# Kernel optimization log

Hardware: AMD Instinct MI355X
Metric: run time of the kernel (lower is better)

Reference implementation:

```python
import jax, jax.numpy as jnp
import numpy as np

N, C, H, W = 4, 256, 64, 64  # in_channels == out_channels == C


def conv1x1(x, w, b):
    # x: [N, Cin, H, W], w: [Cout, Cin], b: [Cout]
    return jnp.einsum('nchw,oc->nohw', x, w) + b[None, :, None, None]


def setup_inputs() -> dict:
    key = jax.random.key(0)
    ks = jax.random.split(key, 4)
    scale = 1.0 / np.sqrt(C)
    return {
        'x': jax.random.normal(ks[0], (N, C, H, W), dtype=jnp.float32),
        'theta_w': jax.random.normal(ks[1], (C, C), dtype=jnp.float32) * scale,
        'theta_b': jnp.zeros((C,), dtype=jnp.float32),
        'phi_w': jax.random.normal(ks[2], (C, C), dtype=jnp.float32) * scale,
        'phi_b': jnp.zeros((C,), dtype=jnp.float32),
        'conv1_w': jax.random.normal(ks[3], (C, C), dtype=jnp.float32) * scale,
        'conv1_b': jnp.zeros((C,), dtype=jnp.float32),
    }


def reference(x, theta_w, theta_b, phi_w, phi_b, conv1_w, conv1_b):
    n, c, h, w = x.shape
    hw = h * w
    theta = conv1x1(x, theta_w, theta_b).reshape(n, c, hw)   # queries [N,C,HW]
    phi = conv1x1(x, phi_w, phi_b).reshape(n, c, hw)         # keys    [N,C,HW]
    g = x.reshape(n, c, hw)                                   # values  [N,C,HW]
    # f = einsum('niab,nicd->nabcd') flattened: [N, HW_q, HW_k]
    scores = jnp.einsum('ncp,ncq->npq', theta, phi) / jnp.sqrt(jnp.asarray(c, x.dtype))
    attn = jax.nn.softmax(scores, axis=-1)                    # softmax over keys
    # f = einsum('nabcd,nicd->niab'): weighted sum of values
    f = jnp.einsum('npq,ncq->ncp', attn, g).reshape(n, c, h, w)
    result = conv1x1(f, conv1_w, conv1_b)
    return x + result
```

## Files before the change

kernel.cpp:

```cpp
#include <hip/hip_runtime.h>
#include <hip/hip_bf16.h>

typedef __attribute__((ext_vector_type(8))) short short8;
typedef __attribute__((ext_vector_type(4))) short short4_t;
typedef __attribute__((ext_vector_type(4))) float float4_t;
typedef unsigned short ushort;

#define HW 4096
#define CC 256
#define NBATCH 4
#define SEQ ((size_t)NBATCH * HW)

static __device__ __forceinline__ unsigned short f2b(float f) {
    union { float f; unsigned u; } v; v.f = f;
    unsigned r = v.u + 0x7FFF + ((v.u >> 16) & 1);
    return (unsigned short)(r >> 16);
}
static __device__ __forceinline__ float b2f(unsigned short u) {
    union { unsigned u; float f; } v; v.u = ((unsigned)u) << 16;
    return v.f;
}
static __device__ __forceinline__ unsigned pk2(float a, float b) {
    __hip_bfloat162 h = __float22bfloat162_rn(make_float2(a, b));
    union { __hip_bfloat162 h; unsigned u; } v; v.h = h; return v.u;
}

__global__ __launch_bounds__(512)
void k_pp(const float* __restrict__ x,
          const float* __restrict__ tw, const float* __restrict__ pw,
          const float* __restrict__ thb, const float* __restrict__ phb,
          unsigned short* __restrict__ gb,
          unsigned short* __restrict__ thT, unsigned short* __restrict__ phT) {
    __shared__ float T[64][65];
    __shared__ __align__(16) ushort F[64][256];
    const int n = blockIdx.z;
    const int p0 = blockIdx.x * 64;
    const int tid = threadIdx.x;

    {
        const int pl = tid & 63, rg = tid >> 6;
        for (int cc = 0; cc < 4; cc++) {
            const int c0 = cc * 64;
            const float* xp = x + ((size_t)n * CC + c0) * HW + p0;
            #pragma unroll
            for (int i = 0; i < 8; i++) {
                int cl = rg * 8 + i;
                float v = xp[(size_t)cl * HW + pl];
                T[cl][pl] = v;
                gb[((size_t)n * CC + c0 + cl) * HW + p0 + pl] = f2b(v);
            }
            __syncthreads();
            const int cl2 = tid & 63, pg = tid >> 6;
            #pragma unroll
            for (int i = 0; i < 8; i++) {
                int plw = pg * 8 + i;
                int c = c0 + cl2;
                int swz = (c >> 3) ^ (plw & 7);
                F[plw][swz * 8 + (c & 7)] = f2b(T[cl2][plw]);
            }
            __syncthreads();
        }
    }

    const int w = tid >> 6, lane = tid & 63;
    const int nidx = lane & 15, quad = lane >> 4;
    const float* Wsel = (w < 4) ? tw : pw;
    const float* bsel = (w < 4) ? thb : phb;
    unsigned short* osel = (w < 4) ? thT : phT;
    const int cq = w & 3;

    float4_t acc[4][4];
    #pragma unroll
    for (int i = 0; i < 4; i++)
        #pragma unroll
        for (int j = 0; j < 4; j++) acc[i][j] = (float4_t)(0.f);

    for (int ks = 0; ks < 8; ks++) {
        short8 af[4];
        #pragma unroll
        for (int mt = 0; mt < 4; mt++) {
            int row = mt * 16 + nidx;
            int chn = (ks * 4 + quad) ^ (row & 7);
            af[mt] = *(const short8*)(&F[row][chn * 8]);
        }
        #pragma unroll
        for (int cb = 0; cb < 4; cb++) {
            int co = cq * 64 + cb * 16 + nidx;
            const float* wp = Wsel + (size_t)co * CC + ks * 32 + quad * 8;
            float4_t w0 = *(const float4_t*)(wp);
            float4_t w1 = *(const float4_t*)(wp + 4);
            union { short8 s; unsigned u[4]; } bfr;
            bfr.u[0] = pk2(w0[0], w0[1]); bfr.u[1] = pk2(w0[2], w0[3]);
            bfr.u[2] = pk2(w1[0], w1[1]); bfr.u[3] = pk2(w1[2], w1[3]);
            #pragma unroll
            for (int mt = 0; mt < 4; mt++)
                acc[mt][cb] = __builtin_amdgcn_mfma_f32_16x16x32_bf16(af[mt], bfr.s, acc[mt][cb], 0, 0, 0);
        }
    }

    #pragma unroll
    for (int cb = 0; cb < 4; cb++) {
        int co = cq * 64 + cb * 16 + nidx;
        float bias = bsel[co];
        #pragma unroll
        for (int mt = 0; mt < 4; mt++)
            #pragma unroll
            for (int r = 0; r < 4; r++) {
                size_t prow = (size_t)n * HW + p0 + mt * 16 + quad * 4 + r;
                osel[prow * CC + co] = f2b(acc[mt][cb][r] + bias);
            }
    }
}

__global__ __launch_bounds__(512)
void k_attn(const unsigned short* __restrict__ thetaT,
            const unsigned short* __restrict__ phiT,
            const unsigned short* __restrict__ gb,
            ushort* __restrict__ Ow, float* __restrict__ lw) {
    __shared__ __align__(16) ushort Kl[2][16384];
    __shared__ __align__(16) ushort Pbuf[2][16][64][8];
    __shared__ float Lbuf[2][128];

    const int tid = threadIdx.x;
    const int w = tid >> 6, lane = tid & 63;
    const int nidx = lane & 15, quad = lane >> 4;
    const int qg = w & 3;
    const int kh = w >> 2;
    const int nb = (blockIdx.x & 7) >> 1;
    const int h  = blockIdx.x & 1;
    const int qtile = blockIdx.x >> 3;
    const int p0 = qtile * 128;
    const size_t seq0 = (size_t)nb * HW;
    const ushort* Kg = phiT + seq0 * CC;
    const ushort* Vg = gb + (size_t)nb * CC * HW;
    const int k00 = h * 2048;

    short8 th[2][8];
    #pragma unroll
    for (int qs = 0; qs < 2; qs++) {
        const ushort* qrow = thetaT + (seq0 + p0 + qg * 32 + qs * 16 + nidx) * CC + quad * 8;
        #pragma unroll
        for (int kb = 0; kb < 8; kb++) th[qs][kb] = *(const short8*)(qrow + kb * 32);
    }

    float4_t o[2][8];
    #pragma unroll
    for (int i = 0; i < 2; i++)
        #pragma unroll
        for (int j = 0; j < 8; j++) o[i][j] = (float4_t)(0.f);
    float lrow[2] = {0.f, 0.f};

    const int c_s = tid >> 4, n_s = tid & 15;
    const int kfbase = (c_s >> 2) * 512 + ((c_s & 3) * 16 + n_s) * 8;
    auto loadKregs = [&](short8 (&kr)[4], int tt) {
        #pragma unroll
        for (int rr = 0; rr < 4; rr++)
            kr[rr] = *(const short8*)(Kg + (size_t)(k00 + tt * 64 + rr * 16 + n_s) * CC + c_s * 8);
    };
    auto stageK = [&](int buf, const short8 (&kr)[4]) {
        #pragma unroll
        for (int rr = 0; rr < 4; rr++) *(short8*)(&Kl[buf][rr * 4096 + kfbase]) = kr[rr];
    };
    auto loadVregs = [&](short8 (&vr)[4], int tt) {
        #pragma unroll
        for (int mg = 0; mg < 2; mg++)
            #pragma unroll
            for (int kst = 0; kst < 2; kst++)
                vr[mg * 2 + kst] = *(const short8*)(Vg + (size_t)(w * 32 + mg * 16 + nidx) * HW
                                                    + k00 + tt * 64 + kst * 32 + quad * 8);
    };

    const float SC = 0.0625f * 1.44269504088896f;
    const int Gp = quad >> 1;
    const int pcell_lo = (nidx ^ (Gp * 4));
    const int pj0 = (quad & 1) * 4;
    const int prcell = ((lane >> 4) << 4) | ((lane & 15) ^ (((lane >> 4) & 1) * 4));

    float4_t s00, s01, s10, s11;
    auto expPhase = [&](int buf) {
        {
            float e0 = exp2f(s00[0] * SC), e1 = exp2f(s00[1] * SC);
            float e2 = exp2f(s00[2] * SC), e3 = exp2f(s00[3] * SC);
            lrow[0] += (e0 + e1) + (e2 + e3);
            uint2 pk; pk.x = pk2(e0, e1); pk.y = pk2(e2, e3);
            *(uint2*)(&Pbuf[buf][(qg * 2 + 0) * 2 + kh][(0 * 2 + Gp) * 16 + pcell_lo][pj0]) = pk;
        }
        {
            float e0 = exp2f(s01[0] * SC), e1 = exp2f(s01[1] * SC);
            float e2 = exp2f(s01[2] * SC), e3 = exp2f(s01[3] * SC);
            lrow[1] += (e0 + e1) + (e2 + e3);
            uint2 pk; pk.x = pk2(e0, e1); pk.y = pk2(e2, e3);
            *(uint2*)(&Pbuf[buf][(qg * 2 + 1) * 2 + kh][(0 * 2 + Gp) * 16 + pcell_lo][pj0]) = pk;
        }
        {
            float e0 = exp2f(s10[0] * SC), e1 = exp2f(s10[1] * SC);
            float e2 = exp2f(s10[2] * SC), e3 = exp2f(s10[3] * SC);
            lrow[0] += (e0 + e1) + (e2 + e3);
            uint2 pk; pk.x = pk2(e0, e1); pk.y = pk2(e2, e3);
            *(uint2*)(&Pbuf[buf][(qg * 2 + 0) * 2 + kh][(1 * 2 + Gp) * 16 + pcell_lo][pj0]) = pk;
        }
        {
            float e0 = exp2f(s11[0] * SC), e1 = exp2f(s11[1] * SC);
            float e2 = exp2f(s11[2] * SC), e3 = exp2f(s11[3] * SC);
            lrow[1] += (e0 + e1) + (e2 + e3);
            uint2 pk; pk.x = pk2(e0, e1); pk.y = pk2(e2, e3);
            *(uint2*)(&Pbuf[buf][(qg * 2 + 1) * 2 + kh][(1 * 2 + Gp) * 16 + pcell_lo][pj0]) = pk;
        }
    };

    short8 kregs[4], vA[4], vB[4];

    auto ITER = [&](int t, const short8 (&vCur)[4], short8 (&vNext)[4]) {
        const int pb = t & 1;
        const int kbuf = (t + 1) & 1;
        s00 = (float4_t)(0.f); s01 = (float4_t)(0.f);
        s10 = (float4_t)(0.f); s11 = (float4_t)(0.f);
        #pragma unroll
        for (int i = 0; i < 8; i++) {
            short8 k0 = *(const short8*)(&Kl[kbuf][((kh * 2 + 0) * 8 + i) * 512 + lane * 8]);
            short8 k1 = *(const short8*)(&Kl[kbuf][((kh * 2 + 1) * 8 + i) * 512 + lane * 8]);
            s00 = __builtin_amdgcn_mfma_f32_16x16x32_bf16(k0, th[0][i], s00, 0, 0, 0);
            s01 = __builtin_amdgcn_mfma_f32_16x16x32_bf16(k0, th[1][i], s01, 0, 0, 0);
            s10 = __builtin_amdgcn_mfma_f32_16x16x32_bf16(k1, th[0][i], s10, 0, 0, 0);
            s11 = __builtin_amdgcn_mfma_f32_16x16x32_bf16(k1, th[1][i], s11, 0, 0, 0);
            short8 pf0 = *(const short8*)(&Pbuf[pb][i * 2 + 0][prcell][0]);
            short8 pf1 = *(const short8*)(&Pbuf[pb][i * 2 + 1][prcell][0]);
            o[0][i] = __builtin_amdgcn_mfma_f32_16x16x32_bf16(vCur[0], pf0, o[0][i], 0, 0, 0);
            o[0][i] = __builtin_amdgcn_mfma_f32_16x16x32_bf16(vCur[1], pf1, o[0][i], 0, 0, 0);
            o[1][i] = __builtin_amdgcn_mfma_f32_16x16x32_bf16(vCur[2], pf0, o[1][i], 0, 0, 0);
            o[1][i] = __builtin_amdgcn_mfma_f32_16x16x32_bf16(vCur[3], pf1, o[1][i], 0, 0, 0);
        }
        loadVregs(vNext, t + 1);
        expPhase((t + 1) & 1);
        if (t < 30) {
            stageK((t + 2) & 1, kregs);
            loadKregs(kregs, (t + 3 < 32) ? t + 3 : 31);
        }
        __syncthreads();
    };

    loadKregs(kregs, 0); loadVregs(vA, 0);
    stageK(0, kregs);
    loadKregs(kregs, 1);
    __syncthreads();
    s00 = (float4_t)(0.f); s01 = (float4_t)(0.f); s10 = (float4_t)(0.f); s11 = (float4_t)(0.f);
    #pragma unroll
    for (int kb = 0; kb < 8; kb++) {
        short8 k0 = *(const short8*)(&Kl[0][((kh * 2 + 0) * 8 + kb) * 512 + lane * 8]);
        short8 k1 = *(const short8*)(&Kl[0][((kh * 2 + 1) * 8 + kb) * 512 + lane * 8]);
        s00 = __builtin_amdgcn_mfma_f32_16x16x32_bf16(k0, th[0][kb], s00, 0, 0, 0);
        s01 = __builtin_amdgcn_mfma_f32_16x16x32_bf16(k0, th[1][kb], s01, 0, 0, 0);
        s10 = __builtin_amdgcn_mfma_f32_16x16x32_bf16(k1, th[0][kb], s10, 0, 0, 0);
        s11 = __builtin_amdgcn_mfma_f32_16x16x32_bf16(k1, th[1][kb], s11, 0, 0, 0);
    }
    expPhase(0);
    stageK(1, kregs);
    loadKregs(kregs, 2);
    __syncthreads();

    #pragma unroll 1
    for (int tt = 0; tt < 15; tt++) {
        ITER(tt * 2, vA, vB);
        ITER(tt * 2 + 1, vB, vA);
    }
    ITER(30, vA, vB);
    #pragma unroll
    for (int i = 0; i < 8; i++) {
        short8 pf0 = *(const short8*)(&Pbuf[1][i * 2 + 0][prcell][0]);
        short8 pf1 = *(const short8*)(&Pbuf[1][i * 2 + 1][prcell][0]);
        o[0][i] = __builtin_amdgcn_mfma_f32_16x16x32_bf16(vB[0], pf0, o[0][i], 0, 0, 0);
        o[0][i] = __builtin_amdgcn_mfma_f32_16x16x32_bf16(vB[1], pf1, o[0][i], 0, 0, 0);
        o[1][i] = __builtin_amdgcn_mfma_f32_16x16x32_bf16(vB[2], pf0, o[1][i], 0, 0, 0);
        o[1][i] = __builtin_amdgcn_mfma_f32_16x16x32_bf16(vB[3], pf1, o[1][i], 0, 0, 0);
    }

    #pragma unroll
    for (int qs = 0; qs < 2; qs++) {
        float v = lrow[qs];
        v += __shfl_xor(v, 16);
        v += __shfl_xor(v, 32);
        if (quad == 0) Lbuf[kh][qg * 32 + qs * 16 + nidx] = v;
    }
    __syncthreads();
    if (tid < 128)
        lw[(size_t)h * SEQ + seq0 + p0 + tid] = Lbuf[0][tid] + Lbuf[1][tid];
    ushort* Op = Ow + ((size_t)h * SEQ + seq0 + p0) * CC;
    #pragma unroll
    for (int mg = 0; mg < 2; mg++)
        #pragma unroll
        for (int qq = 0; qq < 8; qq++) {
            uint2 pk;
            pk.x = pk2(o[mg][qq][0], o[mg][qq][1]);
            pk.y = pk2(o[mg][qq][2], o[mg][qq][3]);
            *(uint2*)(Op + (size_t)(qq * 16 + nidx) * CC + w * 32 + mg * 16 + quad * 4) = pk;
        }
}

__global__ __launch_bounds__(512)
void k_final(const float* __restrict__ cw,
             const float* __restrict__ bc,
             const ushort* __restrict__ Ow,
             const float* __restrict__ lw,
             const float* __restrict__ x,
             float* __restrict__ out) {
    __shared__ __align__(16) ushort F[64][256];
    const int n = blockIdx.z;
    const int p0 = blockIdx.x * 64;
    const int tid = threadIdx.x;

    {
        const int r = tid >> 3;
        const int c0 = tid & 7;
        const size_t grow = (size_t)n * HW + p0 + r;
        const float li = 1.0f / (lw[grow] + lw[SEQ + grow]);
        const short8* O0 = (const short8*)(Ow + grow * CC);
        const short8* O1 = (const short8*)(Ow + SEQ * CC + grow * CC);
        #pragma unroll
        for (int i = 0; i < 4; i++) {
            int ch = c0 + 8 * i;
            short8 a = O0[ch];
            short8 b = O1[ch];
            union { short8 s; unsigned u[4]; } pk;
            float f[8];
            #pragma unroll
            for (int j = 0; j < 8; j++)
                f[j] = (b2f((ushort)a[j]) + b2f((ushort)b[j])) * li;
            pk.u[0] = pk2(f[0], f[1]); pk.u[1] = pk2(f[2], f[3]);
            pk.u[2] = pk2(f[4], f[5]); pk.u[3] = pk2(f[6], f[7]);
            int swz = ch ^ (r & 7);
            *(short8*)(&F[r][swz * 8]) = pk.s;
        }
    }
    __syncthreads();

    const int w = tid >> 6, lane = tid & 63;
    const int nidx = lane & 15, quad = lane >> 4;
    const int co_base = w * 32;
    float4_t acc[2][4];
    #pragma unroll
    for (int i = 0; i < 2; i++)
        #pragma unroll
        for (int j = 0; j < 4; j++) acc[i][j] = (float4_t)(0.f);

    const float* a0row = cw + (size_t)(co_base + nidx) * CC + quad * 8;
    const float* a1row = cw + (size_t)(co_base + 16 + nidx) * CC + quad * 8;
    for (int ks = 0; ks < 8; ks++) {
        float4_t w00 = *(const float4_t*)(a0row + ks * 32);
        float4_t w01 = *(const float4_t*)(a0row + ks * 32 + 4);
        float4_t w10 = *(const float4_t*)(a1row + ks * 32);
        float4_t w11 = *(const float4_t*)(a1row + ks * 32 + 4);
        union { short8 s; unsigned u[4]; } a0, a1;
        a0.u[0] = pk2(w00[0], w00[1]); a0.u[1] = pk2(w00[2], w00[3]);
        a0.u[2] = pk2(w01[0], w01[1]); a0.u[3] = pk2(w01[2], w01[3]);
        a1.u[0] = pk2(w10[0], w10[1]); a1.u[1] = pk2(w10[2], w10[3]);
        a1.u[2] = pk2(w11[0], w11[1]); a1.u[3] = pk2(w11[2], w11[3]);
        #pragma unroll
        for (int pb = 0; pb < 4; pb++) {
            int row = pb * 16 + nidx;
            int chunk = (ks * 4 + quad) ^ (row & 7);
            short8 bb = *(const short8*)(&F[row][chunk * 8]);
            acc[0][pb] = __builtin_amdgcn_mfma_f32_16x16x32_bf16(a0.s, bb, acc[0][pb], 0, 0, 0);
            acc[1][pb] = __builtin_amdgcn_mfma_f32_16x16x32_bf16(a1.s, bb, acc[1][pb], 0, 0, 0);
        }
    }

    #pragma unroll
    for (int cb = 0; cb < 2; cb++) {
        #pragma unroll
        for (int pb = 0; pb < 4; pb++) {
            #pragma unroll
            for (int r2 = 0; r2 < 4; r2++) {
                int co = co_base + cb * 16 + quad * 4 + r2;
                size_t idx = ((size_t)n * CC + co) * HW + p0 + pb * 16 + nidx;
                out[idx] = x[idx] + bc[co] + acc[cb][pb][r2];
            }
        }
    }
}

extern "C" void kernel_launch(void* const* d_in, const int* in_sizes, int n_in,
                              void* d_out, int out_size, void* d_ws, size_t ws_size,
                              hipStream_t stream) {
    const float* x       = (const float*)d_in[0];
    const float* theta_w = (const float*)d_in[1];
    const float* theta_b = (const float*)d_in[2];
    const float* phi_w   = (const float*)d_in[3];
    const float* phi_b   = (const float*)d_in[4];
    const float* conv1_w = (const float*)d_in[5];
    const float* conv1_b = (const float*)d_in[6];
    float* out = (float*)d_out;

    unsigned short* gb  = (unsigned short*)d_ws;
    unsigned short* thT = gb  + SEQ * CC;
    unsigned short* phT = thT + SEQ * CC;
    unsigned short* Ow  = phT + SEQ * CC;
    float* lw = (float*)(Ow + 2 * SEQ * CC);

    k_pp<<<dim3(64, 1, 4), 512, 0, stream>>>(x, theta_w, phi_w, theta_b, phi_b, gb, thT, phT);
    k_attn<<<dim3(256), 512, 0, stream>>>(thT, phT, gb, Ow, lw);
    k_final<<<dim3(64, 1, 4), 512, 0, stream>>>(conv1_w, conv1_b, Ow, lw, x, out);
}
```

Before: 185.1 us.

## Merge three kernels into one cooperative kernel with grid syncs

```diff
diff --git a/kernel.cpp b/kernel.cpp
--- a/kernel.cpp
+++ b/kernel.cpp
@@ -1,8 +1,10 @@
 #include <hip/hip_runtime.h>
 #include <hip/hip_bf16.h>
+#include <hip/hip_cooperative_groups.h>
+
+namespace cg = cooperative_groups;
 
 typedef __attribute__((ext_vector_type(8))) short short8;
-typedef __attribute__((ext_vector_type(4))) short short4_t;
 typedef __attribute__((ext_vector_type(4))) float float4_t;
 typedef unsigned short ushort;
 
@@ -25,354 +27,373 @@
     union { __hip_bfloat162 h; unsigned u; } v; v.h = h; return v.u;
 }
 
+struct SmemAttn {
+    ushort Kl[2][16384];
+    ushort Pbuf[2][16][64][8];
+    float  Lbuf[2][128];
+};
+struct SmemPp {
+    float  T[64][65];
+    ushort F[64][256];
+};
+struct SmemFin {
+    ushort F[64][256];
+};
+union SmemU {
+    SmemAttn a;
+    SmemPp   p;
+    SmemFin  f;
+};
+
 __global__ __launch_bounds__(512)
-void k_pp(const float* __restrict__ x,
-          const float* __restrict__ tw, const float* __restrict__ pw,
-          const float* __restrict__ thb, const float* __restrict__ phb,
-          unsigned short* __restrict__ gb,
-          unsigned short* __restrict__ thT, unsigned short* __restrict__ phT) {
-    __shared__ float T[64][65];
-    __shared__ __align__(16) ushort F[64][256];
-    const int n = blockIdx.z;
-    const int p0 = blockIdx.x * 64;
+void k_mega(const float* __restrict__ x,
+            const float* __restrict__ tw, const float* __restrict__ pw,
+            const float* __restrict__ thb, const float* __restrict__ phb,
+            const float* __restrict__ cw, const float* __restrict__ cbias,
+            unsigned short* __restrict__ gb,
+            unsigned short* __restrict__ thT, unsigned short* __restrict__ phT,
+            ushort* __restrict__ Ow, float* __restrict__ lw,
+            float* __restrict__ out) {
+    __shared__ __align__(16) SmemU sm;
+    cg::grid_group grid = cg::this_grid();
+    const int bid = blockIdx.x;
     const int tid = threadIdx.x;
 
     {
-        const int pl = tid & 63, rg = tid >> 6;
-        for (int cc = 0; cc < 4; cc++) {
-            const int c0 = cc * 64;
-            const float* xp = x + ((size_t)n * CC + c0) * HW + p0;
-            #pragma unroll
-            for (int i = 0; i < 8; i++) {
-                int cl = rg * 8 + i;
-                float v = xp[(size_t)cl * HW + pl];
-                T[cl][pl] = v;
-                gb[((size_t)n * CC + c0 + cl) * HW + p0 + pl] = f2b(v);
-            }
-            __syncthreads();
-            const int cl2 = tid & 63, pg = tid >> 6;
-            #pragma unroll
-            for (int i = 0; i < 8; i++) {
-                int plw = pg * 8 + i;
-                int c = c0 + cl2;
-                int swz = (c >> 3) ^ (plw & 7);
-                F[plw][swz * 8 + (c & 7)] = f2b(T[cl2][plw]);
-            }
-            __syncthreads();
-        }
-    }
-
-    const int w = tid >> 6, lane = tid & 63;
-    const int nidx = lane & 15, quad = lane >> 4;
-    const float* Wsel = (w < 4) ? tw : pw;
-    const float* bsel = (w < 4) ? thb : phb;
-    unsigned short* osel = (w < 4) ? thT : phT;
-    const int cq = w & 3;
-
-    float4_t acc[4][4];
-    #pragma unroll
-    for (int i = 0; i < 4; i++)
-        #pragma unroll
-        for (int j = 0; j < 4; j++) acc[i][j] = (float4_t)(0.f);
-
-    for (int ks = 0; ks < 8; ks++) {
-        short8 af[4];
-        #pragma unroll
-        for (int mt = 0; mt < 4; mt++) {
-            int row = mt * 16 + nidx;
-            int chn = (ks * 4 + quad) ^ (row & 7);
-            af[mt] = *(const short8*)(&F[row][chn * 8]);
-        }
+        auto& T = sm.p.T;
+        auto& F = sm.p.F;
+        const int n = bid >> 6;
+        const int p0 = (bid & 63) * 64;
+
+        {
+            const int pl = tid & 63, rg = tid >> 6;
+            for (int cc = 0; cc < 4; cc++) {
+                const int c0 = cc * 64;
+                const float* xp = x + ((size_t)n * CC + c0) * HW + p0;
+                #pragma unroll
+                for (int i = 0; i < 8; i++) {
+                    int cl = rg * 8 + i;
+                    float v = xp[(size_t)cl * HW + pl];
+                    T[cl][pl] = v;
+                    gb[((size_t)n * CC + c0 + cl) * HW + p0 + pl] = f2b(v);
+                }
+                __syncthreads();
+                const int cl2 = tid & 63, pg = tid >> 6;
+                #pragma unroll
+                for (int i = 0; i < 8; i++) {
+                    int plw = pg * 8 + i;
+                    int c = c0 + cl2;
+                    int swz = (c >> 3) ^ (plw & 7);
+                    F[plw][swz * 8 + (c & 7)] = f2b(T[cl2][plw]);
+                }
+                __syncthreads();
+            }
+        }
+
+        const int w = tid >> 6, lane = tid & 63;
+        const int nidx = lane & 15, quad = lane >> 4;
+        const float* Wsel = (w < 4) ? tw : pw;
+        const float* bsel = (w < 4) ? thb : phb;
+        unsigned short* osel = (w < 4) ? thT : phT;
+        const int cq = w & 3;
+
+        float4_t acc[4][4];
+        #pragma unroll
+        for (int i = 0; i < 4; i++)
+            #pragma unroll
+            for (int j = 0; j < 4; j++) acc[i][j] = (float4_t)(0.f);
+
+        for (int ks = 0; ks < 8; ks++) {
+            short8 af[4];
+            #pragma unroll
+            for (int mt = 0; mt < 4; mt++) {
+                int row = mt * 16 + nidx;
+                int chn = (ks * 4 + quad) ^ (row & 7);
+                af[mt] = *(const short8*)(&F[row][chn * 8]);
+            }
+            #pragma unroll
+            for (int cb = 0; cb < 4; cb++) {
+                int co = cq * 64 + cb * 16 + nidx;
+                const float* wp = Wsel + (size_t)co * CC + ks * 32 + quad * 8;
+                float4_t w0 = *(const float4_t*)(wp);
+                float4_t w1 = *(const float4_t*)(wp + 4);
+                union { short8 s; unsigned u[4]; } bfr;
+                bfr.u[0] = pk2(w0[0], w0[1]); bfr.u[1] = pk2(w0[2], w0[3]);
+                bfr.u[2] = pk2(w1[0], w1[1]); bfr.u[3] = pk2(w1[2], w1[3]);
+                #pragma unroll
+                for (int mt = 0; mt < 4; mt++)
+                    acc[mt][cb] = __builtin_amdgcn_mfma_f32_16x16x32_bf16(af[mt], bfr.s, acc[mt][cb], 0, 0, 0);
+            }
+        }
+
         #pragma unroll
         for (int cb = 0; cb < 4; cb++) {
             int co = cq * 64 + cb * 16 + nidx;
-            const float* wp = Wsel + (size_t)co * CC + ks * 32 + quad * 8;
-            float4_t w0 = *(const float4_t*)(wp);
-            float4_t w1 = *(const float4_t*)(wp + 4);
-            union { short8 s; unsigned u[4]; } bfr;
-            bfr.u[0] = pk2(w0[0], w0[1]); bfr.u[1] = pk2(w0[2], w0[3]);
-            bfr.u[2] = pk2(w1[0], w1[1]); bfr.u[3] = pk2(w1[2], w1[3]);
+            float bias = bsel[co];
             #pragma unroll
             for (int mt = 0; mt < 4; mt++)
-                acc[mt][cb] = __builtin_amdgcn_mfma_f32_16x16x32_bf16(af[mt], bfr.s, acc[mt][cb], 0, 0, 0);
+                #pragma unroll
+                for (int r = 0; r < 4; r++) {
+                    size_t prow = (size_t)n * HW + p0 + mt * 16 + quad * 4 + r;
+                    osel[prow * CC + co] = f2b(acc[mt][cb][r] + bias);
+                }
         }
     }
 
-    #pragma unroll
-    for (int cb = 0; cb < 4; cb++) {
-        int co = cq * 64 + cb * 16 + nidx;
-        float bias = bsel[co];
-        #pragma unroll
-        for (int mt = 0; mt < 4; mt++)
-            #pragma unroll
-            for (int r = 0; r < 4; r++) {
-                size_t prow = (size_t)n * HW + p0 + mt * 16 + quad * 4 + r;
-                osel[prow * CC + co] = f2b(acc[mt][cb][r] + bias);
+    grid.sync();
+
+    {
+        auto& Kl = sm.a.Kl;
+        auto& Pbuf = sm.a.Pbuf;
+        auto& Lbuf = sm.a.Lbuf;
+
+        const int w = tid >> 6, lane = tid & 63;
+        const int nidx = lane & 15, quad = lane >> 4;
+        const int qg = w & 3;
+        const int kh = w >> 2;
+        const int nb = (bid & 7) >> 1;
+        const int h  = bid & 1;
+        const int qtile = bid >> 3;
+        const int p0 = qtile * 128;
+        const size_t seq0 = (size_t)nb * HW;
+        const ushort* Kg = phT + seq0 * CC;
+        const ushort* Vg = gb + (size_t)nb * CC * HW;
+        const int k00 = h * 2048;
+
+        short8 th[2][8];
+        #pragma unroll
+        for (int qs = 0; qs < 2; qs++) {
+            const ushort* qrow = thT + (seq0 + p0 + qg * 32 + qs * 16 + nidx) * CC + quad * 8;
+            #pragma unroll
+            for (int kb = 0; kb < 8; kb++) th[qs][kb] = *(const short8*)(qrow + kb * 32);
+        }
+
+        float4_t o[2][8];
+        #pragma unroll
+        for (int i = 0; i < 2; i++)
+            #pragma unroll
+            for (int j = 0; j < 8; j++) o[i][j] = (float4_t)(0.f);
+        float lrow[2] = {0.f, 0.f};
+
+        const int c_s = tid >> 4, n_s = tid & 15;
+        const int kfbase = (c_s >> 2) * 512 + ((c_s & 3) * 16 + n_s) * 8;
+        auto loadKregs = [&](short8 (&kr)[4], int tt) {
+            #pragma unroll
+            for (int rr = 0; rr < 4; rr++)
+                kr[rr] = *(const short8*)(Kg + (size_t)(k00 + tt * 64 + rr * 16 + n_s) * CC + c_s * 8);
+        };
+        auto stageK = [&](int buf, const short8 (&kr)[4]) {
+            #pragma unroll
+            for (int rr = 0; rr < 4; rr++) *(short8*)(&Kl[buf][rr * 4096 + kfbase]) = kr[rr];
+        };
+        auto loadVregs = [&](short8 (&vr)[4], int tt) {
+            #pragma unroll
+            for (int mg = 0; mg < 2; mg++)
+                #pragma unroll
+                for (int kst = 0; kst < 2; kst++)
+                    vr[mg * 2 + kst] = *(const short8*)(Vg + (size_t)(w * 32 + mg * 16 + nidx) * HW
+                                                        + k00 + tt * 64 + kst * 32 + quad * 8);
+        };
+
+        const float SC = 0.0625f * 1.44269504088896f;
+        const int Gp = quad >> 1;
+        const int pcell_lo = (nidx ^ (Gp * 4));
+        const int pj0 = (quad & 1) * 4;
+        const int prcell = ((lane >> 4) << 4) | ((lane & 15) ^ (((lane >> 4) & 1) * 4));
+
+        float4_t s00, s01, s10, s11;
+        auto expPhase = [&](int buf) {
+            {
+                float e0 = exp2f(s00[0] * SC), e1 = exp2f(s00[1] * SC);
+                float e2 = exp2f(s00[2] * SC), e3 = exp2f(s00[3] * SC);
+                lrow[0] += (e0 + e1) + (e2 + e3);
+                uint2 pk; pk.x = pk2(e0, e1); pk.y = pk2(e2, e3);
+                *(uint2*)(&Pbuf[buf][(qg * 2 + 0) * 2 + kh][(0 * 2 + Gp) * 16 + pcell_lo][pj0]) = pk;
+            }
+            {
+                float e0 = exp2f(s01[0] * SC), e1 = exp2f(s01[1] * SC);
+                float e2 = exp2f(s01[2] * SC), e3 = exp2f(s01[3] * SC);
+                lrow[1] += (e0 + e1) + (e2 + e3);
+                uint2 pk; pk.x = pk2(e0, e1); pk.y = pk2(e2, e3);
+                *(uint2*)(&Pbuf[buf][(qg * 2 + 1) * 2 + kh][(0 * 2 + Gp) * 16 + pcell_lo][pj0]) = pk;
+            }
+            {
+                float e0 = exp2f(s10[0] * SC), e1 = exp2f(s10[1] * SC);
+                float e2 = exp2f(s10[2] * SC), e3 = exp2f(s10[3] * SC);
+                lrow[0] += (e0 + e1) + (e2 + e3);
+                uint2 pk; pk.x = pk2(e0, e1); pk.y = pk2(e2, e3);
+                *(uint2*)(&Pbuf[buf][(qg * 2 + 0) * 2 + kh][(1 * 2 + Gp) * 16 + pcell_lo][pj0]) = pk;
+            }
+            {
+                float e0 = exp2f(s11[0] * SC), e1 = exp2f(s11[1] * SC);
+                float e2 = exp2f(s11[2] * SC), e3 = exp2f(s11[3] * SC);
+                lrow[1] += (e0 + e1) + (e2 + e3);
+                uint2 pk; pk.x = pk2(e0, e1); pk.y = pk2(e2, e3);
+                *(uint2*)(&Pbuf[buf][(qg * 2 + 1) * 2 + kh][(1 * 2 + Gp) * 16 + pcell_lo][pj0]) = pk;
+            }
+        };
+
+        short8 kregs[4], vA[4], vB[4];
+
+        auto ITER = [&](int t, const short8 (&vCur)[4], short8 (&vNext)[4]) {
+            const int pb = t & 1;
+            const int kbuf = (t + 1) & 1;
+            s00 = (float4_t)(0.f); s01 = (float4_t)(0.f);
+            s10 = (float4_t)(0.f); s11 = (float4_t)(0.f);
+            #pragma unroll
+            for (int i = 0; i < 8; i++) {
+                short8 k0 = *(const short8*)(&Kl[kbuf][((kh * 2 + 0) * 8 + i) * 512 + lane * 8]);
+                short8 k1 = *(const short8*)(&Kl[kbuf][((kh * 2 + 1) * 8 + i) * 512 + lane * 8]);
+                s00 = __builtin_amdgcn_mfma_f32_16x16x32_bf16(k0, th[0][i], s00, 0, 0, 0);
+                s01 = __builtin_amdgcn_mfma_f32_16x16x32_bf16(k0, th[1][i], s01, 0, 0, 0);
+                s10 = __builtin_amdgcn_mfma_f32_16x16x32_bf16(k1, th[0][i], s10, 0, 0, 0);
+                s11 = __builtin_amdgcn_mfma_f32_16x16x32_bf16(k1, th[1][i], s11, 0, 0, 0);
+                short8 pf0 = *(const short8*)(&Pbuf[pb][i * 2 + 0][prcell][0]);
+                short8 pf1 = *(const short8*)(&Pbuf[pb][i * 2 + 1][prcell][0]);
+                o[0][i] = __builtin_amdgcn_mfma_f32_16x16x32_bf16(vCur[0], pf0, o[0][i], 0, 0, 0);
+                o[0][i] = __builtin_amdgcn_mfma_f32_16x16x32_bf16(vCur[1], pf1, o[0][i], 0, 0, 0);
+                o[1][i] = __builtin_amdgcn_mfma_f32_16x16x32_bf16(vCur[2], pf0, o[1][i], 0, 0, 0);
+                o[1][i] = __builtin_amdgcn_mfma_f32_16x16x32_bf16(vCur[3], pf1, o[1][i], 0, 0, 0);
+            }
+            loadVregs(vNext, t + 1);
+            expPhase((t + 1) & 1);
+            if (t < 30) {
+                stageK((t + 2) & 1, kregs);
+                loadKregs(kregs, (t + 3 < 32) ? t + 3 : 31);
+            }
+            __syncthreads();
+        };
+
+        loadKregs(kregs, 0); loadVregs(vA, 0);
+        stageK(0, kregs);
+        loadKregs(kregs, 1);
+        __syncthreads();
+        s00 = (float4_t)(0.f); s01 = (float4_t)(0.f); s10 = (float4_t)(0.f); s11 = (float4_t)(0.f);
+        #pragma unroll
+        for (int kb = 0; kb < 8; kb++) {
+            short8 k0 = *(const short8*)(&Kl[0][((kh * 2 + 0) * 8 + kb) * 512 + lane * 8]);
+            short8 k1 = *(const short8*)(&Kl[0][((kh * 2 + 1) * 8 + kb) * 512 + lane * 8]);
+            s00 = __builtin_amdgcn_mfma_f32_16x16x32_bf16(k0, th[0][kb], s00, 0, 0, 0);
+            s01 = __builtin_amdgcn_mfma_f32_16x16x32_bf16(k0, th[1][kb], s01, 0, 0, 0);
+            s10 = __builtin_amdgcn_mfma_f32_16x16x32_bf16(k1, th[0][kb], s10, 0, 0, 0);
+            s11 = __builtin_amdgcn_mfma_f32_16x16x32_bf16(k1, th[1][kb], s11, 0, 0, 0);
+        }
+        expPhase(0);
+        stageK(1, kregs);
+        loadKregs(kregs, 2);
+        __syncthreads();
+
+        #pragma unroll 1
+        for (int tt = 0; tt < 15; tt++) {
+            ITER(tt * 2, vA, vB);
+            ITER(tt * 2 + 1, vB, vA);
+        }
+        ITER(30, vA, vB);
+        #pragma unroll
+        for (int i = 0; i < 8; i++) {
+            short8 pf0 = *(const short8*)(&Pbuf[1][i * 2 + 0][prcell][0]);
+            short8 pf1 = *(const short8*)(&Pbuf[1][i * 2 + 1][prcell][0]);
+            o[0][i] = __builtin_amdgcn_mfma_f32_16x16x32_bf16(vB[0], pf0, o[0][i], 0, 0, 0);
+            o[0][i] = __builtin_amdgcn_mfma_f32_16x16x32_bf16(vB[1], pf1, o[0][i], 0, 0, 0);
+            o[1][i] = __builtin_amdgcn_mfma_f32_16x16x32_bf16(vB[2], pf0, o[1][i], 0, 0, 0);
+            o[1][i] = __builtin_amdgcn_mfma_f32_16x16x32_bf16(vB[3], pf1, o[1][i], 0, 0, 0);
+        }
+
+        #pragma unroll
+        for (int qs = 0; qs < 2; qs++) {
+            float v = lrow[qs];
+            v += __shfl_xor(v, 16);
+            v += __shfl_xor(v, 32);
+            if (quad == 0) Lbuf[kh][qg * 32 + qs * 16 + nidx] = v;
+        }
+        __syncthreads();
+        if (tid < 128)
+            lw[(size_t)h * SEQ + seq0 + p0 + tid] = Lbuf[0][tid] + Lbuf[1][tid];
+        ushort* Op = Ow + ((size_t)h * SEQ + seq0 + p0) * CC;
+        #pragma unroll
+        for (int mg = 0; mg < 2; mg++)
+            #pragma unroll
+            for (int qq = 0; qq < 8; qq++) {
+                uint2 pk;
+                pk.x = pk2(o[mg][qq][0], o[mg][qq][1]);
+                pk.y = pk2(o[mg][qq][2], o[mg][qq][3]);
+                *(uint2*)(Op + (size_t)(qq * 16 + nidx) * CC + w * 32 + mg * 16 + quad * 4) = pk;
             }
     }
-}
-
-__global__ __launch_bounds__(512)
-void k_attn(const unsigned short* __restrict__ thetaT,
-            const unsigned short* __restrict__ phiT,
-            const unsigned short* __restrict__ gb,
-            ushort* __restrict__ Ow, float* __restrict__ lw) {
-    __shared__ __align__(16) ushort Kl[2][16384];
-    __shared__ __align__(16) ushort Pbuf[2][16][64][8];
-    __shared__ float Lbuf[2][128];
-
-    const int tid = threadIdx.x;
-    const int w = tid >> 6, lane = tid & 63;
-    const int nidx = lane & 15, quad = lane >> 4;
-    const int qg = w & 3;
-    const int kh = w >> 2;
-    const int nb = (blockIdx.x & 7) >> 1;
-    const int h  = blockIdx.x & 1;
-    const int qtile = blockIdx.x >> 3;
-    const int p0 = qtile * 128;
-    const size_t seq0 = (size_t)nb * HW;
-    const ushort* Kg = phiT + seq0 * CC;
-    const ushort* Vg = gb + (size_t)nb * CC * HW;
-    const int k00 = h * 2048;
-
-    short8 th[2][8];
-    #pragma unroll
-    for (int qs = 0; qs < 2; qs++) {
-        const ushort* qrow = thetaT + (seq0 + p0 + qg * 32 + qs * 16 + nidx) * CC + quad * 8;
-        #pragma unroll
-        for (int kb = 0; kb < 8; kb++) th[qs][kb] = *(const short8*)(qrow + kb * 32);
-    }
-
-    float4_t o[2][8];
-    #pragma unroll
-    for (int i = 0; i < 2; i++)
-        #pragma unroll
-        for (int j = 0; j < 8; j++) o[i][j] = (float4_t)(0.f);
-    float lrow[2] = {0.f, 0.f};
-
-    const int c_s = tid >> 4, n_s = tid & 15;
-    const int kfbase = (c_s >> 2) * 512 + ((c_s & 3) * 16 + n_s) * 8;
-    auto loadKregs = [&](short8 (&kr)[4], int tt) {
-        #pragma unroll
-        for (int rr = 0; rr < 4; rr++)
-            kr[rr] = *(const short8*)(Kg + (size_t)(k00 + tt * 64 + rr * 16 + n_s) * CC + c_s * 8);
-    };
-    auto stageK = [&](int buf, const short8 (&kr)[4]) {
-        #pragma unroll
-        for (int rr = 0; rr < 4; rr++) *(short8*)(&Kl[buf][rr * 4096 + kfbase]) = kr[rr];
-    };
-    auto loadVregs = [&](short8 (&vr)[4], int tt) {
-        #pragma unroll
-        for (int mg = 0; mg < 2; mg++)
-            #pragma unroll
-            for (int kst = 0; kst < 2; kst++)
-                vr[mg * 2 + kst] = *(const short8*)(Vg + (size_t)(w * 32 + mg * 16 + nidx) * HW
-                                                    + k00 + tt * 64 + kst * 32 + quad * 8);
-    };
-
-    const float SC = 0.0625f * 1.44269504088896f;
-    const int Gp = quad >> 1;
-    const int pcell_lo = (nidx ^ (Gp * 4));
-    const int pj0 = (quad & 1) * 4;
-    const int prcell = ((lane >> 4) << 4) | ((lane & 15) ^ (((lane >> 4) & 1) * 4));
-
-    float4_t s00, s01, s10, s11;
-    auto expPhase = [&](int buf) {
+
+    grid.sync();
+
+    {
+        auto& F = sm.f.F;
+        const int n = bid >> 6;
+        const int p0 = (bid & 63) * 64;
+
         {
-            float e0 = exp2f(s00[0] * SC), e1 = exp2f(s00[1] * SC);
-            float e2 = exp2f(s00[2] * SC), e3 = exp2f(s00[3] * SC);
-            lrow[0] += (e0 + e1) + (e2 + e3);
-            uint2 pk; pk.x = pk2(e0, e1); pk.y = pk2(e2, e3);
-            *(uint2*)(&Pbuf[buf][(qg * 2 + 0) * 2 + kh][(0 * 2 + Gp) * 16 + pcell_lo][pj0]) = pk;
-        }
-        {
-            float e0 = exp2f(s01[0] * SC), e1 = exp2f(s01[1] * SC);
-            float e2 = exp2f(s01[2] * SC), e3 = exp2f(s01[3] * SC);
-            lrow[1] += (e0 + e1) + (e2 + e3);
-            uint2 pk; pk.x = pk2(e0, e1); pk.y = pk2(e2, e3);
-            *(uint2*)(&Pbuf[buf][(qg * 2 + 1) * 2 + kh][(0 * 2 + Gp) * 16 + pcell_lo][pj0]) = pk;
-        }
-        {
-            float e0 = exp2f(s10[0] * SC), e1 = exp2f(s10[1] * SC);
-            float e2 = exp2f(s10[2] * SC), e3 = exp2f(s10[3] * SC);
-            lrow[0] += (e0 + e1) + (e2 + e3);
-            uint2 pk; pk.x = pk2(e0, e1); pk.y = pk2(e2, e3);
-            *(uint2*)(&Pbuf[buf][(qg * 2 + 0) * 2 + kh][(1 * 2 + Gp) * 16 + pcell_lo][pj0]) = pk;
-        }
-        {
-            float e0 = exp2f(s11[0] * SC), e1 = exp2f(s11[1] * SC);
-            float e2 = exp2f(s11[2] * SC), e3 = exp2f(s11[3] * SC);
-            lrow[1] += (e0 + e1) + (e2 + e3);
-            uint2 pk; pk.x = pk2(e0, e1); pk.y = pk2(e2, e3);
-            *(uint2*)(&Pbuf[buf][(qg * 2 + 1) * 2 + kh][(1 * 2 + Gp) * 16 + pcell_lo][pj0]) = pk;
-        }
-    };
-
-    short8 kregs[4], vA[4], vB[4];
-
-    auto ITER = [&](int t, const short8 (&vCur)[4], short8 (&vNext)[4]) {
-        const int pb = t & 1;
-        const int kbuf = (t + 1) & 1;
-        s00 = (float4_t)(0.f); s01 = (float4_t)(0.f);
-        s10 = (float4_t)(0.f); s11 = (float4_t)(0.f);
-        #pragma unroll
-        for (int i = 0; i < 8; i++) {
-            short8 k0 = *(const short8*)(&Kl[kbuf][((kh * 2 + 0) * 8 + i) * 512 + lane * 8]);
-            short8 k1 = *(const short8*)(&Kl[kbuf][((kh * 2 + 1) * 8 + i) * 512 + lane * 8]);
-            s00 = __builtin_amdgcn_mfma_f32_16x16x32_bf16(k0, th[0][i], s00, 0, 0, 0);
-            s01 = __builtin_amdgcn_mfma_f32_16x16x32_bf16(k0, th[1][i], s01, 0, 0, 0);
-            s10 = __builtin_amdgcn_mfma_f32_16x16x32_bf16(k1, th[0][i], s10, 0, 0, 0);
-            s11 = __builtin_amdgcn_mfma_f32_16x16x32_bf16(k1, th[1][i], s11, 0, 0, 0);
-            short8 pf0 = *(const short8*)(&Pbuf[pb][i * 2 + 0][prcell][0]);
-            short8 pf1 = *(const short8*)(&Pbuf[pb][i * 2 + 1][prcell][0]);
-            o[0][i] = __builtin_amdgcn_mfma_f32_16x16x32_bf16(vCur[0], pf0, o[0][i], 0, 0, 0);
-            o[0][i] = __builtin_amdgcn_mfma_f32_16x16x32_bf16(vCur[1], pf1, o[0][i], 0, 0, 0);
-            o[1][i] = __builtin_amdgcn_mfma_f32_16x16x32_bf16(vCur[2], pf0, o[1][i], 0, 0, 0);
-            o[1][i] = __builtin_amdgcn_mfma_f32_16x16x32_bf16(vCur[3], pf1, o[1][i], 0, 0, 0);
-        }
-        loadVregs(vNext, t + 1);
-        expPhase((t + 1) & 1);
-        if (t < 30) {
-            stageK((t + 2) & 1, kregs);
-            loadKregs(kregs, (t + 3 < 32) ? t + 3 : 31);
+            const int r = tid >> 3;
+            const int c0 = tid & 7;
+            const size_t grow = (size_t)n * HW + p0 + r;
+            const float li = 1.0f / (lw[grow] + lw[SEQ + grow]);
+            const short8* O0 = (const short8*)(Ow + grow * CC);
+            const short8* O1 = (const short8*)(Ow + SEQ * CC + grow * CC);
+            #pragma unroll
+            for (int i = 0; i < 4; i++) {
+                int ch = c0 + 8 * i;
+                short8 a = O0[ch];
+                short8 b = O1[ch];
+                union { short8 s; unsigned u[4]; } pk;
+                float f[8];
+                #pragma unroll
+                for (int j = 0; j < 8; j++)
+                    f[j] = (b2f((ushort)a[j]) + b2f((ushort)b[j])) * li;
+                pk.u[0] = pk2(f[0], f[1]); pk.u[1] = pk2(f[2], f[3]);
+                pk.u[2] = pk2(f[4], f[5]); pk.u[3] = pk2(f[6], f[7]);
+                int swz = ch ^ (r & 7);
+                *(short8*)(&F[r][swz * 8]) = pk.s;
+            }
         }
         __syncthreads();
-    };
-
-    loadKregs(kregs, 0); loadVregs(vA, 0);
-    stageK(0, kregs);
-    loadKregs(kregs, 1);
-    __syncthreads();
-    s00 = (float4_t)(0.f); s01 = (float4_t)(0.f); s10 = (float4_t)(0.f); s11 = (float4_t)(0.f);
-    #pragma unroll
-    for (int kb = 0; kb < 8; kb++) {
-        short8 k0 = *(const short8*)(&Kl[0][((kh * 2 + 0) * 8 + kb) * 512 + lane * 8]);
-        short8 k1 = *(const short8*)(&Kl[0][((kh * 2 + 1) * 8 + kb) * 512 + lane * 8]);
-        s00 = __builtin_amdgcn_mfma_f32_16x16x32_bf16(k0, th[0][kb], s00, 0, 0, 0);
-        s01 = __builtin_amdgcn_mfma_f32_16x16x32_bf16(k0, th[1][kb], s01, 0, 0, 0);
-        s10 = __builtin_amdgcn_mfma_f32_16x16x32_bf16(k1, th[0][kb], s10, 0, 0, 0);
-        s11 = __builtin_amdgcn_mfma_f32_16x16x32_bf16(k1, th[1][kb], s11, 0, 0, 0);
-    }
-    expPhase(0);
-    stageK(1, kregs);
-    loadKregs(kregs, 2);
-    __syncthreads();
-
-    #pragma unroll 1
-    for (int tt = 0; tt < 15; tt++) {
-        ITER(tt * 2, vA, vB);
-        ITER(tt * 2 + 1, vB, vA);
-    }
-    ITER(30, vA, vB);
-    #pragma unroll
-    for (int i = 0; i < 8; i++) {
-        short8 pf0 = *(const short8*)(&Pbuf[1][i * 2 + 0][prcell][0]);
-        short8 pf1 = *(const short8*)(&Pbuf[1][i * 2 + 1][prcell][0]);
-        o[0][i] = __builtin_amdgcn_mfma_f32_16x16x32_bf16(vB[0], pf0, o[0][i], 0, 0, 0);
-        o[0][i] = __builtin_amdgcn_mfma_f32_16x16x32_bf16(vB[1], pf1, o[0][i], 0, 0, 0);
-        o[1][i] = __builtin_amdgcn_mfma_f32_16x16x32_bf16(vB[2], pf0, o[1][i], 0, 0, 0);
-        o[1][i] = __builtin_amdgcn_mfma_f32_16x16x32_bf16(vB[3], pf1, o[1][i], 0, 0, 0);
-    }
-
-    #pragma unroll
-    for (int qs = 0; qs < 2; qs++) {
-        float v = lrow[qs];
-        v += __shfl_xor(v, 16);
-        v += __shfl_xor(v, 32);
-        if (quad == 0) Lbuf[kh][qg * 32 + qs * 16 + nidx] = v;
-    }
-    __syncthreads();
-    if (tid < 128)
-        lw[(size_t)h * SEQ + seq0 + p0 + tid] = Lbuf[0][tid] + Lbuf[1][tid];
-    ushort* Op = Ow + ((size_t)h * SEQ + seq0 + p0) * CC;
-    #pragma unroll
-    for (int mg = 0; mg < 2; mg++)
-        #pragma unroll
-        for (int qq = 0; qq < 8; qq++) {
-            uint2 pk;
-            pk.x = pk2(o[mg][qq][0], o[mg][qq][1]);
-            pk.y = pk2(o[mg][qq][2], o[mg][qq][3]);
-            *(uint2*)(Op + (size_t)(qq * 16 + nidx) * CC + w * 32 + mg * 16 + quad * 4) = pk;
-        }
-}
-
-__global__ __launch_bounds__(512)
-void k_final(const float* __restrict__ cw,
-             const float* __restrict__ bc,
-             const ushort* __restrict__ Ow,
-             const float* __restrict__ lw,
-             const float* __restrict__ x,
-             float* __restrict__ out) {
-    __shared__ __align__(16) ushort F[64][256];
-    const int n = blockIdx.z;
-    const int p0 = blockIdx.x * 64;
-    const int tid = threadIdx.x;
-
-    {
-        const int r = tid >> 3;
-        const int c0 = tid & 7;
-        const size_t grow = (size_t)n * HW + p0 + r;
-        const float li = 1.0f / (lw[grow] + lw[SEQ + grow]);
-        const short8* O0 = (const short8*)(Ow + grow * CC);
-        const short8* O1 = (const short8*)(Ow + SEQ * CC + grow * CC);
-        #pragma unroll
-        for (int i = 0; i < 4; i++) {
-            int ch = c0 + 8 * i;
-            short8 a = O0[ch];
-            short8 b = O1[ch];
-            union { short8 s; unsigned u[4]; } pk;
-            float f[8];
-            #pragma unroll
-            for (int j = 0; j < 8; j++)
-                f[j] = (b2f((ushort)a[j]) + b2f((ushort)b[j])) * li;
-            pk.u[0] = pk2(f[0], f[1]); pk.u[1] = pk2(f[2], f[3]);
-            pk.u[2] = pk2(f[4], f[5]); pk.u[3] = pk2(f[6], f[7]);
-            int swz = ch ^ (r & 7);
-            *(short8*)(&F[r][swz * 8]) = pk.s;
-        }
-    }
-    __syncthreads();
-
-    const int w = tid >> 6, lane = tid & 63;
-    const int nidx = lane & 15, quad = lane >> 4;
-    const int co_base = w * 32;
-    float4_t acc[2][4];
-    #pragma unroll
-    for (int i = 0; i < 2; i++)
-        #pragma unroll
-        for (int j = 0; j < 4; j++) acc[i][j] = (float4_t)(0.f);
-
-    const float* a0row = cw + (size_t)(co_base + nidx) * CC + quad * 8;
-    const float* a1row = cw + (size_t)(co_base + 16 + nidx) * CC + quad * 8;
-    for (int ks = 0; ks < 8; ks++) {
-        float4_t w00 = *(const float4_t*)(a0row + ks * 32);
-        float4_t w01 = *(const float4_t*)(a0row + ks * 32 + 4);
-        float4_t w10 = *(const float4_t*)(a1row + ks * 32);
-        float4_t w11 = *(const float4_t*)(a1row + ks * 32 + 4);
-        union { short8 s; unsigned u[4]; } a0, a1;
-        a0.u[0] = pk2(w00[0], w00[1]); a0.u[1] = pk2(w00[2], w00[3]);
-        a0.u[2] = pk2(w01[0], w01[1]); a0.u[3] = pk2(w01[2], w01[3]);
-        a1.u[0] = pk2(w10[0], w10[1]); a1.u[1] = pk2(w10[2], w10[3]);
-        a1.u[2] = pk2(w11[0], w11[1]); a1.u[3] = pk2(w11[2], w11[3]);
-        #pragma unroll
-        for (int pb = 0; pb < 4; pb++) {
-            int row = pb * 16 + nidx;
-            int chunk = (ks * 4 + quad) ^ (row & 7);
-            short8 bb = *(const short8*)(&F[row][chunk * 8]);
-            acc[0][pb] = __builtin_amdgcn_mfma_f32_16x16x32_bf16(a0.s, bb, acc[0][pb], 0, 0, 0);
-            acc[1][pb] = __builtin_amdgcn_mfma_f32_16x16x32_bf16(a1.s, bb, acc[1][pb], 0, 0, 0);
-        }
-    }
-
-    #pragma unroll
-    for (int cb = 0; cb < 2; cb++) {
-        #pragma unroll
-        for (int pb = 0; pb < 4; pb++) {
-            #pragma unroll
-            for (int r2 = 0; r2 < 4; r2++) {
-                int co = co_base + cb * 16 + quad * 4 + r2;
-                size_t idx = ((size_t)n * CC + co) * HW + p0 + pb * 16 + nidx;
-                out[idx] = x[idx] + bc[co] + acc[cb][pb][r2];
+
+        const int w = tid >> 6, lane = tid & 63;
+        const int nidx = lane & 15, quad = lane >> 4;
+        const int co_base = w * 32;
+        float4_t acc[2][4];
+        #pragma unroll
+        for (int i = 0; i < 2; i++)
+            #pragma unroll
+            for (int j = 0; j < 4; j++) acc[i][j] = (float4_t)(0.f);
+
+        const float* a0row = cw + (size_t)(co_base + nidx) * CC + quad * 8;
+        const float* a1row = cw + (size_t)(co_base + 16 + nidx) * CC + quad * 8;
+        for (int ks = 0; ks < 8; ks++) {
+            float4_t w00 = *(const float4_t*)(a0row + ks * 32);
+            float4_t w01 = *(const float4_t*)(a0row + ks * 32 + 4);
+            float4_t w10 = *(const float4_t*)(a1row + ks * 32);
+            float4_t w11 = *(const float4_t*)(a1row + ks * 32 + 4);
+            union { short8 s; unsigned u[4]; } a0, a1;
+            a0.u[0] = pk2(w00[0], w00[1]); a0.u[1] = pk2(w00[2], w00[3]);
+            a0.u[2] = pk2(w01[0], w01[1]); a0.u[3] = pk2(w01[2], w01[3]);
+            a1.u[0] = pk2(w10[0], w10[1]); a1.u[1] = pk2(w10[2], w10[3]);
+            a1.u[2] = pk2(w11[0], w11[1]); a1.u[3] = pk2(w11[2], w11[3]);
+            #pragma unroll
+            for (int pb = 0; pb < 4; pb++) {
+                int row = pb * 16 + nidx;
+                int chunk = (ks * 4 + quad) ^ (row & 7);
+                short8 bb = *(const short8*)(&F[row][chunk * 8]);
+                acc[0][pb] = __builtin_amdgcn_mfma_f32_16x16x32_bf16(a0.s, bb, acc[0][pb], 0, 0, 0);
+                acc[1][pb] = __builtin_amdgcn_mfma_f32_16x16x32_bf16(a1.s, bb, acc[1][pb], 0, 0, 0);
+            }
+        }
+
+        #pragma unroll
+        for (int cb = 0; cb < 2; cb++) {
+            #pragma unroll
+            for (int pb = 0; pb < 4; pb++) {
+                #pragma unroll
+                for (int r2 = 0; r2 < 4; r2++) {
+                    int co = co_base + cb * 16 + quad * 4 + r2;
+                    size_t idx = ((size_t)n * CC + co) * HW + p0 + pb * 16 + nidx;
+                    out[idx] = x[idx] + cbias[co] + acc[cb][pb][r2];
+                }
             }
         }
     }
@@ -396,7 +417,10 @@
     unsigned short* Ow  = phT + SEQ * CC;
     float* lw = (float*)(Ow + 2 * SEQ * CC);
 
-    k_pp<<<dim3(64, 1, 4), 512, 0, stream>>>(x, theta_w, phi_w, theta_b, phi_b, gb, thT, phT);
-    k_attn<<<dim3(256), 512, 0, stream>>>(thT, phT, gb, Ow, lw);
-    k_final<<<dim3(64, 1, 4), 512, 0, stream>>>(conv1_w, conv1_b, Ow, lw, x, out);
+    void* kargs[] = {
+        (void*)&x, (void*)&theta_w, (void*)&phi_w, (void*)&theta_b, (void*)&phi_b,
+        (void*)&conv1_w, (void*)&conv1_b,
+        (void*)&gb, (void*)&thT, (void*)&phT, (void*)&Ow, (void*)&lw, (void*)&out
+    };
+    hipLaunchCooperativeKernel((void*)k_mega, dim3(256), dim3(512), kargs, 0, stream);
 }
```

Result: slower. 286.7 us (+54.9%).
